# Performance work log

Measured on AMD Instinct MI355X. Metric: run time of the kernel, lower is better.

## Reference

```python
import jax, jax.numpy as jnp
import numpy as np

N_MESS = 50000
MAX_NEI = 8
INPUT_SIZE = 128
H_SIZE = 128
DEPTH = 5


def setup_inputs() -> dict:
    key = jax.random.key(0)
    ks = jax.random.split(key, 7)
    s = 0.05
    fmess = jax.random.normal(ks[0], (N_MESS, INPUT_SIZE), dtype=jnp.float32)
    bgraph = jax.random.randint(ks[1], (N_MESS, MAX_NEI), 0, N_MESS, dtype=jnp.int32)
    # torch nn.Linear weights are [out_features, in_features]
    W_z = jax.random.normal(ks[2], (H_SIZE, INPUT_SIZE + H_SIZE), dtype=jnp.float32) * s
    b_z = jnp.zeros((H_SIZE,), jnp.float32)
    W_r = jax.random.normal(ks[3], (H_SIZE, INPUT_SIZE), dtype=jnp.float32) * s  # no bias
    U_r = jax.random.normal(ks[4], (H_SIZE, H_SIZE), dtype=jnp.float32) * s
    b_Ur = jnp.zeros((H_SIZE,), jnp.float32)
    W_h = jax.random.normal(ks[5], (H_SIZE, INPUT_SIZE + H_SIZE), dtype=jnp.float32) * s
    b_h = jnp.zeros((H_SIZE,), jnp.float32)
    return {"fmess": fmess, "bgraph": bgraph, "W_z": W_z, "b_z": b_z,
            "W_r": W_r, "U_r": U_r, "b_Ur": b_Ur, "W_h": W_h, "b_h": b_h}


def _gru_step(fmess, h_nei, W_z, b_z, W_r, U_r, b_Ur, W_h, b_h):
    # h_nei: [N, K, H]
    sum_h = h_nei.sum(axis=1)                                     # [N, H]
    z = jax.nn.sigmoid(jnp.concatenate([fmess, sum_h], axis=1) @ W_z.T + b_z)
    r_1 = (fmess @ W_r.T)[:, None, :]                             # [N, 1, H]
    r_2 = jnp.einsum('nkh,gh->nkg', h_nei, U_r) + b_Ur            # [N, K, H]
    r = jax.nn.sigmoid(r_1 + r_2)
    sum_gated_h = (r * h_nei).sum(axis=1)                         # [N, H]
    pre_h = jnp.tanh(jnp.concatenate([fmess, sum_gated_h], axis=1) @ W_h.T + b_h)
    return (1.0 - z) * sum_h + z * pre_h


def reference(fmess, bgraph, W_z, b_z, W_r, U_r, b_Ur, W_h, b_h):
    n = fmess.shape[0]
    h = jnp.zeros((n, H_SIZE), dtype=fmess.dtype)
    mask = jnp.ones((n, 1), dtype=fmess.dtype).at[0, 0].set(0.0)  # message 0 is padding
    for _ in range(DEPTH):
        h_nei = h[bgraph]                                         # gather: [N, K, H]
        h = _gru_step(fmess, h_nei, W_z, b_z, W_r, U_r, b_Ur, W_h, b_h)
        h = h * mask
    return h
```

## Files before the change

kernel.cpp:

```cpp
#include <hip/hip_runtime.h>
#include <hip/hip_bf16.h>

#define NM 50000
#define HD 128
#define KNEI 8
#define BM 64
#define SPAD 136
#define NBLK ((NM + BM - 1) / BM)
#define NH ((size_t)NM * (size_t)HD)
#define FRAG 8192

typedef float  fx4   __attribute__((ext_vector_type(4)));
typedef short  s16x8 __attribute__((ext_vector_type(8)));
typedef short  s16x4 __attribute__((ext_vector_type(4)));

__device__ __forceinline__ float sigm_f(float x) {
    return __builtin_amdgcn_rcpf(1.0f + __expf(-x));
}
__device__ __forceinline__ float tanh_f(float x) {
    return 2.0f * sigm_f(2.0f * x) - 1.0f;
}
__device__ __forceinline__ unsigned short f2b(float f) {
    __hip_bfloat16 h = __float2bfloat16(f);
    return __builtin_bit_cast(unsigned short, h);
}
__device__ __forceinline__ float b2f(unsigned short u) {
    __hip_bfloat16 h = __builtin_bit_cast(__hip_bfloat16, u);
    return __bfloat162float(h);
}

#define MFMA16(a, b, c) __builtin_amdgcn_mfma_f32_16x16x32_bf16(a, b, c, 0, 0, 0)


__device__ __forceinline__ void stage_W16(const unsigned short* __restrict__ W16,
                                          int ldw, int woff,
                                          unsigned short (*Ws)[SPAD], int tid)
{
    const int g  = tid >> 1;
    const int c0 = (tid & 1) << 6;
    const unsigned short* src = W16 + (size_t)g * ldw + woff + c0;
    #pragma unroll
    for (int j = 0; j < 64; j += 8)
        *(s16x8*)&Ws[g][c0 + j] = *(const s16x8*)(src + j);
}

__device__ __forceinline__ void stage_A32(const float* __restrict__ A, int row0,
                                          unsigned short (*As)[SPAD], int tid)
{
    const int r  = tid & 63;
    const int c0 = (tid >> 6) << 5;
    int gr = row0 + r; if (gr >= NM) gr = NM - 1;
    const float* ap = A + (size_t)gr * HD + c0;
    #pragma unroll
    for (int j = 0; j < 32; j += 8) {
        s16x8 s;
        #pragma unroll
        for (int q = 0; q < 8; ++q) s[q] = (short)f2b(ap[j + q]);
        *(s16x8*)&As[r][c0 + j] = s;
    }
}

__device__ __forceinline__ void stage_A16(const unsigned short* __restrict__ A16, int row0,
                                          unsigned short (*As)[SPAD], int tid)
{
    const int r  = tid & 63;
    const int c0 = (tid >> 6) << 5;
    int gr = row0 + r; if (gr >= NM) gr = NM - 1;
    const unsigned short* ap = A16 + (size_t)gr * HD + c0;
    #pragma unroll
    for (int j = 0; j < 32; j += 8)
        *(s16x8*)&As[r][c0 + j] = *(const s16x8*)(ap + j);
}

__device__ __forceinline__ void lds_to_g16(const unsigned short (*L)[SPAD], int row0,
                                           unsigned short* __restrict__ G, int tid)
{
    const int r  = tid & 63;
    const int c0 = (tid >> 6) << 5;
    const int gr = row0 + r;
    if (gr >= NM) return;
    #pragma unroll
    for (int j = 0; j < 32; j += 8)
        *(s16x8*)&G[(size_t)gr * HD + c0 + j] = *(const s16x8*)&L[r][c0 + j];
}

__device__ __forceinline__ void mfma_128(const unsigned short (*As)[SPAD],
                                         const unsigned short (*Ws)[SPAD],
                                         int w, int l, fx4 (&acc)[8])
{
    const int rb = w * 16 + (l & 15);
    const int kq = (l >> 4) << 3;
    #pragma unroll
    for (int ks = 0; ks < 4; ++ks) {
        const s16x8 a = *(const s16x8*)&As[rb][ks * 32 + kq];
        #pragma unroll
        for (int nf = 0; nf < 8; ++nf) {
            const s16x8 b = *(const s16x8*)&Ws[nf * 16 + (l & 15)][ks * 32 + kq];
            acc[nf] = MFMA16(a, b, acc[nf]);
        }
    }
}

#define ZACC(acc) { _Pragma("unroll") for (int z_ = 0; z_ < 8; ++z_) \
                    acc[z_] = (fx4)0.0f; }

__global__ __launch_bounds__(256)
void dgru_wcvt(const float* __restrict__ Wz, const float* __restrict__ Wr,
               const float* __restrict__ Ur, const float* __restrict__ Wh,
               unsigned short* __restrict__ w16)
{
    const int i = blockIdx.x * 256 + threadIdx.x;
    float v;
    if      (i < 32768) v = Wz[i];
    else if (i < 49152) v = Wr[i - 32768];
    else if (i < 65536) v = Ur[i - 49152];
    else                v = Wh[i - 65536];
    w16[i] = f2b(v);
}

__global__ __launch_bounds__(256)
void dgru_pre(const float* __restrict__ fmess,
              const unsigned short* __restrict__ wz16,
              const unsigned short* __restrict__ wr16,
              const unsigned short* __restrict__ wh16,
              const unsigned short* __restrict__ ur16,
              const float* __restrict__ bz, const float* __restrict__ bh,
              const float* __restrict__ bur,
              float* __restrict__ pre_z, float* __restrict__ pre_r,
              float* __restrict__ pre_hf,
              unsigned short* __restrict__ h16, unsigned short* __restrict__ uh16)
{
    __shared__ unsigned short As[BM][SPAD];
    __shared__ unsigned short Ws[HD][SPAD];
    const int tid  = threadIdx.x;
    const int row0 = blockIdx.x * BM;
    const int w    = tid >> 6;
    const int l    = tid & 63;
    const size_t fb = (size_t)blockIdx.x * FRAG + (size_t)w * 2048 + (size_t)l * 4;

    stage_A32(fmess, row0, As, tid);
    stage_W16(wz16, 2 * HD, 0, Ws, tid);
    __syncthreads();

    fx4 accz[8];
    ZACC(accz);
    mfma_128(As, Ws, w, l, accz);
    #pragma unroll
    for (int nf = 0; nf < 8; ++nf) {
        const float bv = bz[nf * 16 + (l & 15)];
        #pragma unroll
        for (int q = 0; q < 4; ++q) accz[nf][q] += bv;
        *(fx4*)&pre_z[fb + nf * 256] = accz[nf];
    }
    __syncthreads();

    stage_W16(wr16, HD, 0, Ws, tid);
    __syncthreads();
    {
        fx4 acc[8]; ZACC(acc);
        mfma_128(As, Ws, w, l, acc);
        #pragma unroll
        for (int nf = 0; nf < 8; ++nf) {
            const int col = nf * 16 + (l & 15);
            #pragma unroll
            for (int q = 0; q < 4; ++q) {
                const int gr = row0 + w * 16 + ((l >> 4) << 2) + q;
                if (gr < NM) pre_r[(size_t)gr * HD + col] = acc[nf][q];
            }
        }
    }
    __syncthreads();

    stage_W16(wh16, 2 * HD, 0, Ws, tid);
    __syncthreads();
    {
        fx4 acc[8]; ZACC(acc);
        mfma_128(As, Ws, w, l, acc);
        __syncthreads();
        #pragma unroll
        for (int nf = 0; nf < 8; ++nf) {
            const int col = nf * 16 + (l & 15);
            const float bv = bh[nf * 16 + (l & 15)];
            fx4 p;
            #pragma unroll
            for (int q = 0; q < 4; ++q) p[q] = acc[nf][q] + bv;
            *(fx4*)&pre_hf[fb + nf * 256] = p;
            #pragma unroll
            for (int q = 0; q < 4; ++q) {
                const int rl = w * 16 + ((l >> 4) << 2) + q;
                const int gr = row0 + rl;
                float h0 = sigm_f(accz[nf][q]) * tanh_f(p[q]);
                if (gr == 0) h0 = 0.0f;
                As[rl][col] = f2b(h0);
            }
        }
    }
    stage_W16(ur16, HD, 0, Ws, tid);
    __syncthreads();

    lds_to_g16(As, row0, h16, tid);
    {
        fx4 acc[8]; ZACC(acc);
        mfma_128(As, Ws, w, l, acc);
        __syncthreads();
        #pragma unroll
        for (int nf = 0; nf < 8; ++nf) {
            const int col = nf * 16 + (l & 15);
            const float bv = bur[nf * 16 + (l & 15)];
            #pragma unroll
            for (int q = 0; q < 4; ++q) {
                const int rl = w * 16 + ((l >> 4) << 2) + q;
                Ws[rl][col] = f2b(acc[nf][q] + bv);
            }
        }
        __syncthreads();
        lds_to_g16(Ws, row0, uh16, tid);
    }
}

__global__ __launch_bounds__(256)
void dgru_gather(const unsigned short* __restrict__ h16,
                 const unsigned short* __restrict__ uh16,
                 const int* __restrict__ bgraph, const float* __restrict__ pre_r,
                 unsigned short* __restrict__ sh16, unsigned short* __restrict__ sg16)
{
    const int tid = threadIdx.x;
    const int n   = blockIdx.x * 8 + (tid >> 5);
    const int d0  = (tid & 31) << 2;

    const int4* bg = (const int4*)(bgraph + (size_t)n * KNEI);
    const int4 b0 = bg[0], b1 = bg[1];
    const int idx[KNEI] = {b0.x, b0.y, b0.z, b0.w, b1.x, b1.y, b1.z, b1.w};

    s16x4 hr[KNEI], ur[KNEI];
    #pragma unroll
    for (int k = 0; k < KNEI; ++k)
        hr[k] = *(const s16x4*)&h16[(size_t)idx[k] * HD + d0];
    #pragma unroll
    for (int k = 0; k < KNEI; ++k)
        ur[k] = *(const s16x4*)&uh16[(size_t)idx[k] * HD + d0];
    const fx4 pr = *(const fx4*)&pre_r[(size_t)n * HD + d0];

    float sh[4] = {0.f, 0.f, 0.f, 0.f};
    float sg[4] = {0.f, 0.f, 0.f, 0.f};
    #pragma unroll
    for (int k = 0; k < KNEI; ++k) {
        #pragma unroll
        for (int j = 0; j < 4; ++j) {
            const float hv = b2f((unsigned short)hr[k][j]);
            const float uv = b2f((unsigned short)ur[k][j]);
            sh[j] += hv;
            sg[j] = fmaf(sigm_f(pr[j] + uv), hv, sg[j]);
        }
    }
    s16x4 osh, osg;
    #pragma unroll
    for (int j = 0; j < 4; ++j) {
        osh[j] = (short)f2b(sh[j]);
        osg[j] = (short)f2b(sg[j]);
    }
    const size_t o = (size_t)n * HD + d0;
    *(s16x4*)&sh16[o] = osh;
    *(s16x4*)&sg16[o] = osg;
}

__global__ __launch_bounds__(256)
void dgru_zh(const unsigned short* __restrict__ sh16,
             const unsigned short* __restrict__ sg16,
             const float* __restrict__ pre_z, const float* __restrict__ pre_hf,
             const unsigned short* __restrict__ wz16,
             const unsigned short* __restrict__ wh16,
             const unsigned short* __restrict__ ur16,
             const float* __restrict__ bur,
             unsigned short* __restrict__ h16, unsigned short* __restrict__ uh16,
             float* __restrict__ hout, int last)
{
    __shared__ unsigned short AsH[BM][SPAD];
    __shared__ unsigned short AsG[BM][SPAD];
    __shared__ unsigned short Ws[HD][SPAD];
    const int tid  = threadIdx.x;
    const int row0 = blockIdx.x * BM;
    const int w    = tid >> 6;
    const int l    = tid & 63;
    const size_t fb = (size_t)blockIdx.x * FRAG + (size_t)w * 2048 + (size_t)l * 4;

    stage_A16(sh16, row0, AsH, tid);
    stage_A16(sg16, row0, AsG, tid);
    stage_W16(wz16, 2 * HD, HD, Ws, tid);
    __syncthreads();
    fx4 zres[8];
    {
        fx4 acc[8]; ZACC(acc);
        mfma_128(AsH, Ws, w, l, acc);
        #pragma unroll
        for (int nf = 0; nf < 8; ++nf) {
            const fx4 p = *(const fx4*)&pre_z[fb + nf * 256];
            #pragma unroll
            for (int q = 0; q < 4; ++q) zres[nf][q] = sigm_f(p[q] + acc[nf][q]);
        }
    }
    __syncthreads();

    stage_W16(wh16, 2 * HD, HD, Ws, tid);
    __syncthreads();

    {
        fx4 acc[8]; ZACC(acc);
        mfma_128(AsG, Ws, w, l, acc);
        #pragma unroll
        for (int nf = 0; nf < 8; ++nf) {
            const int col = nf * 16 + (l & 15);
            const fx4 p = *(const fx4*)&pre_hf[fb + nf * 256];
            #pragma unroll
            for (int q = 0; q < 4; ++q) {
                const int rl = w * 16 + ((l >> 4) << 2) + q;
                const int gr = row0 + rl;
                const float shv = b2f(AsH[rl][col]);
                const float zz  = zres[nf][q];
                float o = (1.0f - zz) * shv + zz * tanh_f(p[q] + acc[nf][q]);
                if (gr == 0) o = 0.0f;
                if (last) {
                    if (gr < NM) hout[(size_t)gr * HD + col] = o;
                } else {
                    AsH[rl][col] = f2b(o);
                }
            }
        }
    }
    if (last) return;
    __syncthreads();

    stage_W16(ur16, HD, 0, Ws, tid);
    lds_to_g16(AsH, row0, h16, tid);
    __syncthreads();

    {
        fx4 acc[8]; ZACC(acc);
        mfma_128(AsH, Ws, w, l, acc);
        __syncthreads();
        #pragma unroll
        for (int nf = 0; nf < 8; ++nf) {
            const int col = nf * 16 + (l & 15);
            const float bv = bur[nf * 16 + (l & 15)];
            #pragma unroll
            for (int q = 0; q < 4; ++q) {
                const int rl = w * 16 + ((l >> 4) << 2) + q;
                AsG[rl][col] = f2b(acc[nf][q] + bv);
            }
        }
        __syncthreads();
        lds_to_g16(AsG, row0, uh16, tid);
    }
}

extern "C" void kernel_launch(void* const* d_in, const int* in_sizes, int n_in,
                              void* d_out, int out_size, void* d_ws, size_t ws_size,
                              hipStream_t stream) {
    const float* fmess  = (const float*)d_in[0];
    const int*   bgraph = (const int*)  d_in[1];
    const float* W_z    = (const float*)d_in[2];
    const float* b_z    = (const float*)d_in[3];
    const float* W_r    = (const float*)d_in[4];
    const float* U_r    = (const float*)d_in[5];
    const float* b_Ur   = (const float*)d_in[6];
    const float* W_h    = (const float*)d_in[7];
    const float* b_h    = (const float*)d_in[8];

    float* ws = (float*)d_ws;
    const size_t FPAD = (size_t)NBLK * FRAG;
    float* pre_z  = ws;
    float* pre_hf = ws + FPAD;
    float* pre_r  = ws + 2 * FPAD;
    unsigned short* h16  = (unsigned short*)(pre_r + NH);
    unsigned short* uh16 = h16 + NH;
    unsigned short* sh16 = uh16 + NH;
    unsigned short* sg16 = sh16 + NH;
    unsigned short* w16  = sg16 + NH;
    unsigned short* wz16 = w16;
    unsigned short* wr16 = w16 + 32768;
    unsigned short* ur16 = w16 + 49152;
    unsigned short* wh16 = w16 + 65536;
    float* hout = (float*)d_out;

    dgru_wcvt<<<dim3(384), dim3(256), 0, stream>>>(W_z, W_r, U_r, W_h, w16);

    dgru_pre<<<dim3(NBLK), dim3(256), 0, stream>>>(
        fmess, wz16, wr16, wh16, ur16, b_z, b_h, b_Ur,
        pre_z, pre_r, pre_hf, h16, uh16);

    for (int it = 1; it < 5; ++it) {
        dgru_gather<<<dim3(NM / 8), dim3(256), 0, stream>>>(
            h16, uh16, bgraph, pre_r, sh16, sg16);
        dgru_zh<<<dim3(NBLK), dim3(256), 0, stream>>>(
            sh16, sg16, pre_z, pre_hf, wz16, wh16, ur16, b_Ur,
            h16, uh16, hout, (it == 4) ? 1 : 0);
    }
}
```

Before: 330.1 us.

## Recompute fmess projections per step from bf16 fmess instead of storing fp32 pre-activations

Instead of precomputing fmess@W_z and fmess@W_h once and storing them as fp32 fragments read every iteration, the zh kernel now stages a bf16 copy of fmess and recomputes both projections with extra MFMA passes, accumulating them into the same accumulators as the hidden-state part. pre_r is also stored as bf16 instead of fp32. This trades global memory traffic (two fp32 N×128 reads per step) for doubled MFMA work and extra weight staging and barriers per block. Rounding pre_r to bf16 adds some precision loss.

Result: slower. 338.2 us (+2.5%).

```diff
diff --git a/kernel.cpp b/kernel.cpp
--- a/kernel.cpp
+++ b/kernel.cpp
@@ -8,7 +8,6 @@
 #define SPAD 136
 #define NBLK ((NM + BM - 1) / BM)
 #define NH ((size_t)NM * (size_t)HD)
-#define FRAG 8192
 
 typedef float  fx4   __attribute__((ext_vector_type(4)));
 typedef short  s16x8 __attribute__((ext_vector_type(8)));
@@ -126,8 +125,8 @@
               const unsigned short* __restrict__ ur16,
               const float* __restrict__ bz, const float* __restrict__ bh,
               const float* __restrict__ bur,
-              float* __restrict__ pre_z, float* __restrict__ pre_r,
-              float* __restrict__ pre_hf,
+              unsigned short* __restrict__ fmess16,
+              unsigned short* __restrict__ pre_r16,
               unsigned short* __restrict__ h16, unsigned short* __restrict__ uh16)
 {
     __shared__ unsigned short As[BM][SPAD];
@@ -136,60 +135,53 @@
     const int row0 = blockIdx.x * BM;
     const int w    = tid >> 6;
     const int l    = tid & 63;
-    const size_t fb = (size_t)blockIdx.x * FRAG + (size_t)w * 2048 + (size_t)l * 4;
 
     stage_A32(fmess, row0, As, tid);
     stage_W16(wz16, 2 * HD, 0, Ws, tid);
     __syncthreads();
 
-    fx4 accz[8];
-    ZACC(accz);
+    lds_to_g16(As, row0, fmess16, tid);
+
+    fx4 accz[8]; ZACC(accz);
     mfma_128(As, Ws, w, l, accz);
-    #pragma unroll
-    for (int nf = 0; nf < 8; ++nf) {
-        const float bv = bz[nf * 16 + (l & 15)];
-        #pragma unroll
-        for (int q = 0; q < 4; ++q) accz[nf][q] += bv;
-        *(fx4*)&pre_z[fb + nf * 256] = accz[nf];
-    }
     __syncthreads();
 
     stage_W16(wr16, HD, 0, Ws, tid);
     __syncthreads();
     {
-        fx4 acc[8]; ZACC(acc);
-        mfma_128(As, Ws, w, l, acc);
+        fx4 accr[8]; ZACC(accr);
+        mfma_128(As, Ws, w, l, accr);
+        __syncthreads();
         #pragma unroll
         for (int nf = 0; nf < 8; ++nf) {
             const int col = nf * 16 + (l & 15);
             #pragma unroll
             for (int q = 0; q < 4; ++q) {
-                const int gr = row0 + w * 16 + ((l >> 4) << 2) + q;
-                if (gr < NM) pre_r[(size_t)gr * HD + col] = acc[nf][q];
+                const int rl = w * 16 + ((l >> 4) << 2) + q;
+                Ws[rl][col] = f2b(accr[nf][q]);
             }
         }
-    }
-    __syncthreads();
+        __syncthreads();
+        lds_to_g16(Ws, row0, pre_r16, tid);
+        __syncthreads();
+    }
 
     stage_W16(wh16, 2 * HD, 0, Ws, tid);
     __syncthreads();
     {
-        fx4 acc[8]; ZACC(acc);
-        mfma_128(As, Ws, w, l, acc);
+        fx4 acch[8]; ZACC(acch);
+        mfma_128(As, Ws, w, l, acch);
         __syncthreads();
         #pragma unroll
         for (int nf = 0; nf < 8; ++nf) {
             const int col = nf * 16 + (l & 15);
-            const float bv = bh[nf * 16 + (l & 15)];
-            fx4 p;
-            #pragma unroll
-            for (int q = 0; q < 4; ++q) p[q] = acc[nf][q] + bv;
-            *(fx4*)&pre_hf[fb + nf * 256] = p;
+            const float bvz = bz[col];
+            const float bvh = bh[col];
             #pragma unroll
             for (int q = 0; q < 4; ++q) {
                 const int rl = w * 16 + ((l >> 4) << 2) + q;
                 const int gr = row0 + rl;
-                float h0 = sigm_f(accz[nf][q]) * tanh_f(p[q]);
+                float h0 = sigm_f(accz[nf][q] + bvz) * tanh_f(acch[nf][q] + bvh);
                 if (gr == 0) h0 = 0.0f;
                 As[rl][col] = f2b(h0);
             }
@@ -200,17 +192,17 @@
 
     lds_to_g16(As, row0, h16, tid);
     {
-        fx4 acc[8]; ZACC(acc);
-        mfma_128(As, Ws, w, l, acc);
+        fx4 accu[8]; ZACC(accu);
+        mfma_128(As, Ws, w, l, accu);
         __syncthreads();
         #pragma unroll
         for (int nf = 0; nf < 8; ++nf) {
             const int col = nf * 16 + (l & 15);
-            const float bv = bur[nf * 16 + (l & 15)];
+            const float bv = bur[col];
             #pragma unroll
             for (int q = 0; q < 4; ++q) {
                 const int rl = w * 16 + ((l >> 4) << 2) + q;
-                Ws[rl][col] = f2b(acc[nf][q] + bv);
+                Ws[rl][col] = f2b(accu[nf][q] + bv);
             }
         }
         __syncthreads();
@@ -221,7 +213,8 @@
 __global__ __launch_bounds__(256)
 void dgru_gather(const unsigned short* __restrict__ h16,
                  const unsigned short* __restrict__ uh16,
-                 const int* __restrict__ bgraph, const float* __restrict__ pre_r,
+                 const int* __restrict__ bgraph,
+                 const unsigned short* __restrict__ pre_r16,
                  unsigned short* __restrict__ sh16, unsigned short* __restrict__ sg16)
 {
     const int tid = threadIdx.x;
@@ -239,7 +232,10 @@
     #pragma unroll
     for (int k = 0; k < KNEI; ++k)
         ur[k] = *(const s16x4*)&uh16[(size_t)idx[k] * HD + d0];
-    const fx4 pr = *(const fx4*)&pre_r[(size_t)n * HD + d0];
+    const s16x4 prb = *(const s16x4*)&pre_r16[(size_t)n * HD + d0];
+    float pr[4];
+    #pragma unroll
+    for (int j = 0; j < 4; ++j) pr[j] = b2f((unsigned short)prb[j]);
 
     float sh[4] = {0.f, 0.f, 0.f, 0.f};
     float sg[4] = {0.f, 0.f, 0.f, 0.f};
@@ -265,65 +261,76 @@
 }
 
 __global__ __launch_bounds__(256)
-void dgru_zh(const unsigned short* __restrict__ sh16,
+void dgru_zh(const unsigned short* __restrict__ fmess16,
+             const unsigned short* __restrict__ sh16,
              const unsigned short* __restrict__ sg16,
-             const float* __restrict__ pre_z, const float* __restrict__ pre_hf,
              const unsigned short* __restrict__ wz16,
              const unsigned short* __restrict__ wh16,
              const unsigned short* __restrict__ ur16,
+             const float* __restrict__ bz, const float* __restrict__ bh,
              const float* __restrict__ bur,
              unsigned short* __restrict__ h16, unsigned short* __restrict__ uh16,
              float* __restrict__ hout, int last)
 {
-    __shared__ unsigned short AsH[BM][SPAD];
-    __shared__ unsigned short AsG[BM][SPAD];
+    __shared__ unsigned short AsF[BM][SPAD];
+    __shared__ unsigned short AsX[BM][SPAD];
     __shared__ unsigned short Ws[HD][SPAD];
     const int tid  = threadIdx.x;
     const int row0 = blockIdx.x * BM;
     const int w    = tid >> 6;
     const int l    = tid & 63;
-    const size_t fb = (size_t)blockIdx.x * FRAG + (size_t)w * 2048 + (size_t)l * 4;
-
-    stage_A16(sh16, row0, AsH, tid);
-    stage_A16(sg16, row0, AsG, tid);
+
+    stage_A16(fmess16, row0, AsF, tid);
+    stage_A16(sh16, row0, AsX, tid);
+    stage_W16(wz16, 2 * HD, 0, Ws, tid);
+    __syncthreads();
+    fx4 acc[8]; ZACC(acc);
+    mfma_128(AsF, Ws, w, l, acc);
+    __syncthreads();
     stage_W16(wz16, 2 * HD, HD, Ws, tid);
     __syncthreads();
+    mfma_128(AsX, Ws, w, l, acc);
+
     fx4 zres[8];
-    {
-        fx4 acc[8]; ZACC(acc);
-        mfma_128(AsH, Ws, w, l, acc);
-        #pragma unroll
-        for (int nf = 0; nf < 8; ++nf) {
-            const fx4 p = *(const fx4*)&pre_z[fb + nf * 256];
-            #pragma unroll
-            for (int q = 0; q < 4; ++q) zres[nf][q] = sigm_f(p[q] + acc[nf][q]);
-        }
-    }
-    __syncthreads();
-
+    float shv[8][4];
+    #pragma unroll
+    for (int nf = 0; nf < 8; ++nf) {
+        const int col = nf * 16 + (l & 15);
+        const float bv = bz[col];
+        #pragma unroll
+        for (int q = 0; q < 4; ++q) {
+            const int rl = w * 16 + ((l >> 4) << 2) + q;
+            zres[nf][q] = sigm_f(acc[nf][q] + bv);
+            shv[nf][q]  = b2f(AsX[rl][col]);
+        }
+    }
+    __syncthreads();
+
+    stage_A16(sg16, row0, AsX, tid);
+    stage_W16(wh16, 2 * HD, 0, Ws, tid);
+    __syncthreads();
+    ZACC(acc);
+    mfma_128(AsF, Ws, w, l, acc);
+    __syncthreads();
     stage_W16(wh16, 2 * HD, HD, Ws, tid);
     __syncthreads();
-
-    {
-        fx4 acc[8]; ZACC(acc);
-        mfma_128(AsG, Ws, w, l, acc);
-        #pragma unroll
-        for (int nf = 0; nf < 8; ++nf) {
-            const int col = nf * 16 + (l & 15);
-            const fx4 p = *(const fx4*)&pre_hf[fb + nf * 256];
-            #pragma unroll
-            for (int q = 0; q < 4; ++q) {
-                const int rl = w * 16 + ((l >> 4) << 2) + q;
-                const int gr = row0 + rl;
-                const float shv = b2f(AsH[rl][col]);
-                const float zz  = zres[nf][q];
-                float o = (1.0f - zz) * shv + zz * tanh_f(p[q] + acc[nf][q]);
-                if (gr == 0) o = 0.0f;
-                if (last) {
-                    if (gr < NM) hout[(size_t)gr * HD + col] = o;
-                } else {
-                    AsH[rl][col] = f2b(o);
-                }
+    mfma_128(AsX, Ws, w, l, acc);
+
+    #pragma unroll
+    for (int nf = 0; nf < 8; ++nf) {
+        const int col = nf * 16 + (l & 15);
+        const float bv = bh[col];
+        #pragma unroll
+        for (int q = 0; q < 4; ++q) {
+            const int rl = w * 16 + ((l >> 4) << 2) + q;
+            const int gr = row0 + rl;
+            const float zz = zres[nf][q];
+            float o = (1.0f - zz) * shv[nf][q] + zz * tanh_f(acc[nf][q] + bv);
+            if (gr == 0) o = 0.0f;
+            if (last) {
+                if (gr < NM) hout[(size_t)gr * HD + col] = o;
+            } else {
+                AsF[rl][col] = f2b(o);
             }
         }
     }
@@ -331,26 +338,22 @@
     __syncthreads();
 
     stage_W16(ur16, HD, 0, Ws, tid);
-    lds_to_g16(AsH, row0, h16, tid);
-    __syncthreads();
-
-    {
-        fx4 acc[8]; ZACC(acc);
-        mfma_128(AsH, Ws, w, l, acc);
-        __syncthreads();
-        #pragma unroll
-        for (int nf = 0; nf < 8; ++nf) {
-            const int col = nf * 16 + (l & 15);
-            const float bv = bur[nf * 16 + (l & 15)];
-            #pragma unroll
-            for (int q = 0; q < 4; ++q) {
-                const int rl = w * 16 + ((l >> 4) << 2) + q;
-                AsG[rl][col] = f2b(acc[nf][q] + bv);
-            }
-        }
-        __syncthreads();
-        lds_to_g16(AsG, row0, uh16, tid);
-    }
+    lds_to_g16(AsF, row0, h16, tid);
+    __syncthreads();
+    ZACC(acc);
+    mfma_128(AsF, Ws, w, l, acc);
+    #pragma unroll
+    for (int nf = 0; nf < 8; ++nf) {
+        const int col = nf * 16 + (l & 15);
+        const float bv = bur[col];
+        #pragma unroll
+        for (int q = 0; q < 4; ++q) {
+            const int rl = w * 16 + ((l >> 4) << 2) + q;
+            AsX[rl][col] = f2b(acc[nf][q] + bv);
+        }
+    }
+    __syncthreads();
+    lds_to_g16(AsX, row0, uh16, tid);
 }
 
 extern "C" void kernel_launch(void* const* d_in, const int* in_sizes, int n_in,
@@ -366,16 +369,14 @@
     const float* W_h    = (const float*)d_in[7];
     const float* b_h    = (const float*)d_in[8];
 
-    float* ws = (float*)d_ws;
-    const size_t FPAD = (size_t)NBLK * FRAG;
-    float* pre_z  = ws;
-    float* pre_hf = ws + FPAD;
-    float* pre_r  = ws + 2 * FPAD;
-    unsigned short* h16  = (unsigned short*)(pre_r + NH);
-    unsigned short* uh16 = h16 + NH;
-    unsigned short* sh16 = uh16 + NH;
-    unsigned short* sg16 = sh16 + NH;
-    unsigned short* w16  = sg16 + NH;
+    unsigned short* ws16 = (unsigned short*)d_ws;
+    unsigned short* fmess16 = ws16;
+    unsigned short* pre_r16 = ws16 + NH;
+    unsigned short* h16     = ws16 + 2 * NH;
+    unsigned short* uh16    = ws16 + 3 * NH;
+    unsigned short* sh16    = ws16 + 4 * NH;
+    unsigned short* sg16    = ws16 + 5 * NH;
+    unsigned short* w16     = ws16 + 6 * NH;
     unsigned short* wz16 = w16;
     unsigned short* wr16 = w16 + 32768;
     unsigned short* ur16 = w16 + 49152;
@@ -386,13 +387,13 @@
 
     dgru_pre<<<dim3(NBLK), dim3(256), 0, stream>>>(
         fmess, wz16, wr16, wh16, ur16, b_z, b_h, b_Ur,
-        pre_z, pre_r, pre_hf, h16, uh16);
+        fmess16, pre_r16, h16, uh16);
 
     for (int it = 1; it < 5; ++it) {
         dgru_gather<<<dim3(NM / 8), dim3(256), 0, stream>>>(
-            h16, uh16, bgraph, pre_r, sh16, sg16);
+            h16, uh16, bgraph, pre_r16, sh16, sg16);
         dgru_zh<<<dim3(NBLK), dim3(256), 0, stream>>>(
-            sh16, sg16, pre_z, pre_hf, wz16, wh16, ur16, b_Ur,
+            fmess16, sh16, sg16, wz16, wh16, ur16, b_z, b_h, b_Ur,
             h16, uh16, hout, (it == 4) ? 1 : 0);
     }
 }
```
